# Performance work log

Measured on AMD Instinct MI355X. Metric: run time of the kernel, lower is better.

## Reference

```python
import jax, jax.numpy as jnp
import numpy as np

NF, D, H = 32, 256, 128  # n_features, d_model, d_model//2
B, T = 16, 512
EPS = 1e-5

def _ln(x, g, b):
    m = jnp.mean(x, axis=-1, keepdims=True)
    v = jnp.mean((x - m) ** 2, axis=-1, keepdims=True)
    return (x - m) * jax.lax.rsqrt(v + EPS) * g + b


def setup_inputs() -> dict:
    key = jax.random.key(0)
    ks = jax.random.split(key, 16)
    s = 0.05
    inp = {
        "x": jax.random.normal(ks[0], (B, T, NF), dtype=jnp.float32),
        # batched per-feature GRN params (d_in=1 -> fc1 weight is (NF,H))
        "w1": jax.random.normal(ks[1], (NF, H)) * s,
        "b1": jnp.zeros((NF, H)),
        "w2": jax.random.normal(ks[2], (NF, H, D)) * s,
        "b2": jnp.zeros((NF, D)),
        "wg": jax.random.normal(ks[3], (NF, H, D)) * s,
        "bg": jnp.zeros((NF, D)),
        "ws": jax.random.normal(ks[4], (NF, D)) * s,  # skip Linear(1,D)
        "bs": jnp.zeros((NF, D)),
        "ln_g": jnp.ones((NF, D)),
        "ln_b": jnp.zeros((NF, D)),
        # weight GRN: d_in=NF*D, d_hidden=D, d_out=NF
        "W1": jax.random.normal(ks[5], (NF * D, D)) * s,
        "B1": jnp.zeros((D,)),
        "W2": jax.random.normal(ks[6], (D, NF)) * s,
        "B2": jnp.zeros((NF,)),
        "Wg": jax.random.normal(ks[7], (D, NF)) * s,
        "Bg": jnp.zeros((NF,)),
        "Ws": jax.random.normal(ks[8], (NF * D, NF)) * s,
        "Bs": jnp.zeros((NF,)),
        "LN_g": jnp.ones((NF,)),
        "LN_b": jnp.zeros((NF,)),
    }
    return inp


def reference(x, w1, b1, w2, b2, wg, bg, ws, bs, ln_g, ln_b,
              W1, B1, W2, B2, Wg, Bg, Ws, Bs, LN_g, LN_b):
    Bn, Tn, Fn = x.shape
    # --- all per-feature GRNs batched over the feature axis (dropout=eval/identity) ---
    h = jax.nn.elu(x[..., None] * w1 + b1)                      # (B,T,F,H)
    proj = jnp.einsum('btfh,fhd->btfd', h, w2) + b2             # (B,T,F,D)
    gate = jax.nn.sigmoid(jnp.einsum('btfh,fhd->btfd', h, wg) + bg)
    skip = x[..., None] * ws + bs                               # (B,T,F,D)
    stacked = _ln(skip + gate * proj, ln_g, ln_b)               # (B,T,F,D)
    # --- softmax feature weights from mean-pooled flat features ---
    flat_pooled = stacked.mean(axis=1).reshape(Bn, Fn * stacked.shape[-1])  # (B,F*D)
    hw = jax.nn.elu(flat_pooled @ W1 + B1)                      # (B,D)
    pw = hw @ W2 + B2
    gw = jax.nn.sigmoid(hw @ Wg + Bg)
    wgrn = _ln(flat_pooled @ Ws + Bs + gw * pw, LN_g, LN_b)     # (B,F)
    weights = jax.nn.softmax(wgrn, axis=-1)                     # (B,F)
    # --- weighted feature combine ---
    selected = jnp.einsum('btfd,bf->btd', stacked, weights)     # (B,T,D)
    return selected, weights
```

## Files before the change

kernel.cpp:

```cpp
#include <hip/hip_runtime.h>
#include <hip/hip_fp16.h>

#define NF 32
#define DM 256
#define HH 128
#define BB 16
#define TT 512
#define BT 8192
#define OUT_W_OFF 2097152
#define EPS 1e-5f

typedef __bf16 bf16x8 __attribute__((ext_vector_type(8)));
typedef float  f32x16 __attribute__((ext_vector_type(16)));
typedef __fp16 f16x2 __attribute__((ext_vector_type(2)));
typedef __fp16 f16x8 __attribute__((ext_vector_type(8)));

__device__ __forceinline__ float eluf(float z){ return z > 0.f ? z : __expf(z) - 1.f; }
__device__ __forceinline__ float sigm(float z){ return 1.f/(1.f + __expf(-z)); }
__device__ __forceinline__ unsigned f2bf(float x){
  unsigned u = __float_as_uint(x);
  u += 0x7fffu + ((u>>16)&1u);
  return u>>16;
}

template<int MT, int NTHR>
__device__ __forceinline__ void build_A(uint4* Apack, const float* __restrict__ x,
                                        const float* __restrict__ w1, const float* __restrict__ b1,
                                        int f, int tok0, int tid){
  #pragma unroll
  for (int p = 0; p < (MT*512)/NTHR; ++p){
    int slot = tid + p*NTHR;
    int l  = slot & 63;
    int ks = (slot>>6)&7;
    int mt = slot>>9;
    int m  = mt*32 + (l&31);
    int k0 = ks*16 + (l>>5)*8;
    float xv = x[(tok0+m)*NF + f];
    const float* wp = w1 + f*HH + k0;
    const float* bp = b1 + f*HH + k0;
    float4 wa = *(const float4*)wp, wb = *(const float4*)(wp+4);
    float4 ba = *(const float4*)bp, bb = *(const float4*)(bp+4);
    bf16x8 v;
    v[0] = (__bf16)eluf(fmaf(xv, wa.x, ba.x));
    v[1] = (__bf16)eluf(fmaf(xv, wa.y, ba.y));
    v[2] = (__bf16)eluf(fmaf(xv, wa.z, ba.z));
    v[3] = (__bf16)eluf(fmaf(xv, wa.w, ba.w));
    v[4] = (__bf16)eluf(fmaf(xv, wb.x, bb.x));
    v[5] = (__bf16)eluf(fmaf(xv, wb.y, bb.y));
    v[6] = (__bf16)eluf(fmaf(xv, wb.z, bb.z));
    v[7] = (__bf16)eluf(fmaf(xv, wb.w, bb.w));
    Apack[slot] = __builtin_bit_cast(uint4, v);
  }
}

__global__ __launch_bounds__(256) void k_prep(const float* __restrict__ w2,
                                              const float* __restrict__ wgm,
                                              uint4* __restrict__ Wpk){
  __shared__ float ssrc[2][128][32];
  const int tid = threadIdx.x;
  const int f = blockIdx.x, c = blockIdx.y;
  #pragma unroll
  for (int it = 0; it < 32; ++it){
    int idx = tid + it*256;
    int arr = idx >> 12;
    int rem = idx & 4095;
    int k = rem >> 5, dd = rem & 31;
    const float* src = arr ? wgm : w2;
    ssrc[arr][k][dd] = src[(f*HH + k)*DM + c*32 + dd];
  }
  __syncthreads();
  #pragma unroll
  for (int p = 0; p < 4; ++p){
    int oc = tid + p*256;
    int nt = oc>>9, ks = (oc>>6)&7, l = oc&63;
    int k0 = ks*16 + (l>>5)*8, dd = l&31;
    float v[8];
    #pragma unroll
    for (int j=0;j<8;++j) v[j] = ssrc[nt][k0+j][dd];
    uint4 pk;
    pk.x = f2bf(v[0]) | (f2bf(v[1])<<16);
    pk.y = f2bf(v[2]) | (f2bf(v[3])<<16);
    pk.z = f2bf(v[4]) | (f2bf(v[5])<<16);
    pk.w = f2bf(v[6]) | (f2bf(v[7])<<16);
    Wpk[(f*8 + c)*1024 + oc] = pk;
  }
}

__global__ __launch_bounds__(512, 2) void k_pass1(const float* __restrict__ x,  const float* __restrict__ w1,
    const float* __restrict__ b1, const float* __restrict__ b2, const float* __restrict__ bg,
    const float* __restrict__ wsk, const float* __restrict__ bsk,
    const float* __restrict__ lng, const float* __restrict__ lnb,
    const uint4* __restrict__ Wpk,
    float* __restrict__ pooled, uint4* __restrict__ stk4){
  __shared__ uint4 smem[4096];
  __shared__ float xs[128];
  __shared__ float poolbuf[256];
  const int tid = threadIdx.x, lane = tid&63, wid = tid>>6;
  const int tt = wid>>1, ch = wid&1;
  const int col = lane&31, q = lane>>5;
  const int f = blockIdx.y;
  const int tok0 = blockIdx.x*128;
  const int b = tok0 >> 9;
  if (tid < 256) poolbuf[tid] = 0.f;
  if (tid < 128) xs[tid] = x[(tok0 + tid)*NF + f];

  build_A<4,512>(smem, x, w1, b1, f, tok0, tid);
  __syncthreads();
  bf16x8 afr[8];
  #pragma unroll
  for (int ks=0; ks<8; ++ks) afr[ks] = __builtin_bit_cast(bf16x8, smem[(tt*8+ks)*64 + lane]);
  __syncthreads();

  __fp16* stage = (__fp16*)smem;
  #pragma unroll 1
  for (int ci=0; ci<4; ++ci){
    const int c = ch*4 + ci;
    const uint4* wb = Wpk + (f*8 + c)*1024;
    bf16x8 bfr[8];
    #pragma unroll
    for (int ks=0;ks<8;++ks) bfr[ks] = __builtin_bit_cast(bf16x8, wb[ks*64 + lane]);
    f32x16 acc0 = {0.f};
    #pragma unroll
    for (int ks=0;ks<8;++ks) acc0 = __builtin_amdgcn_mfma_f32_32x32x16_bf16(afr[ks], bfr[ks], acc0, 0,0,0);
    __builtin_amdgcn_sched_barrier(0);
    #pragma unroll
    for (int ks=0;ks<8;++ks) bfr[ks] = __builtin_bit_cast(bf16x8, wb[512 + ks*64 + lane]);
    f32x16 acc1 = {0.f};
    #pragma unroll
    for (int ks=0;ks<8;++ks) acc1 = __builtin_amdgcn_mfma_f32_32x32x16_bf16(afr[ks], bfr[ks], acc1, 0,0,0);
    __builtin_amdgcn_sched_barrier(0);
    const int d = c*32 + col;
    const float b2v = b2[f*DM+d], bgv = bg[f*DM+d];
    #pragma unroll
    for (int i=0;i<8;++i){
      const int r0 = 2*i, r1 = r0+1;
      const int t0 = tt*32 + (r0&3) + 8*(i>>1) + 4*q;
      stage[ t0   *256 + d] = (__fp16)(sigm(acc1[r0]+bgv)*(acc0[r0]+b2v));
      stage[(t0+1)*256 + d] = (__fp16)(sigm(acc1[r1]+bgv)*(acc0[r1]+b2v));
    }
  }
  __syncthreads();

  const int oc = tid & 31;
  float4 ga = *(const float4*)(lng + f*DM + oc*8);
  float4 gb = *(const float4*)(lng + f*DM + oc*8 + 4);
  float4 la = *(const float4*)(lnb + f*DM + oc*8);
  float4 lb = *(const float4*)(lnb + f*DM + oc*8 + 4);
  float4 wa = *(const float4*)(wsk + f*DM + oc*8);
  float4 wbv = *(const float4*)(wsk + f*DM + oc*8 + 4);
  float4 sa = *(const float4*)(bsk + f*DM + oc*8);
  float4 sb = *(const float4*)(bsk + f*DM + oc*8 + 4);
  float gj[8] = {ga.x,ga.y,ga.z,ga.w,gb.x,gb.y,gb.z,gb.w};
  float bj[8] = {la.x,la.y,la.z,la.w,lb.x,lb.y,lb.z,lb.w};
  float wj[8] = {wa.x,wa.y,wa.z,wa.w,wbv.x,wbv.y,wbv.z,wbv.w};
  float cj[8] = {sa.x,sa.y,sa.z,sa.w,sb.x,sb.y,sb.z,sb.w};
  float ps[8];
  #pragma unroll
  for (int j=0;j<8;++j) ps[j]=0.f;
  #pragma unroll
  for (int p=0;p<8;++p){
    int slot = tid + p*512;
    int t = slot >> 5;
    uint4 v = smem[slot];
    f16x8 s8 = __builtin_bit_cast(f16x8, v);
    float xt = xs[t];
    float s[8];
    float ssum = 0.f, ssq = 0.f;
    #pragma unroll
    for (int j=0;j<8;++j){
      s[j] = fmaf(xt, wj[j], cj[j]) + (float)s8[j];
      ssum += s[j];
      ssq = fmaf(s[j], s[j], ssq);
    }
    ssum += __shfl_xor(ssum,1);  ssq += __shfl_xor(ssq,1);
    ssum += __shfl_xor(ssum,2);  ssq += __shfl_xor(ssq,2);
    ssum += __shfl_xor(ssum,4);  ssq += __shfl_xor(ssq,4);
    ssum += __shfl_xor(ssum,8);  ssq += __shfl_xor(ssq,8);
    ssum += __shfl_xor(ssum,16); ssq += __shfl_xor(ssq,16);
    float mu = ssum * (1.f/256.f);
    float var = fmaf(-mu, mu, ssq*(1.f/256.f));
    float rs = rsqrtf(fmaxf(var, 0.f) + EPS);
    float nmr = -mu*rs;
    float sh[8];
    #pragma unroll
    for (int j=0;j<8;++j){
      sh[j] = fmaf(fmaf(s[j], rs, nmr), gj[j], bj[j]);
      ps[j] += sh[j];
    }
    uint4 pk;
    pk.x = __builtin_bit_cast(unsigned, __builtin_amdgcn_cvt_pkrtz(sh[0], sh[1]));
    pk.y = __builtin_bit_cast(unsigned, __builtin_amdgcn_cvt_pkrtz(sh[2], sh[3]));
    pk.z = __builtin_bit_cast(unsigned, __builtin_amdgcn_cvt_pkrtz(sh[4], sh[5]));
    pk.w = __builtin_bit_cast(unsigned, __builtin_amdgcn_cvt_pkrtz(sh[6], sh[7]));
    stk4[(size_t)(tok0 + t)*1024 + (size_t)f*32 + oc] = pk;
  }
  #pragma unroll
  for (int j=0;j<8;++j) ps[j] += __shfl_xor(ps[j], 32);
  if (q == 0){
    #pragma unroll
    for (int j=0;j<8;++j) atomicAdd(&poolbuf[oc*8 + j], ps[j]);
  }
  __syncthreads();
  if (tid < 256) atomicAdd(&pooled[b*8192 + f*DM + tid], poolbuf[tid]);
}

__global__ __launch_bounds__(256) void k_pass2a(const float* __restrict__ pooled,
    const float* __restrict__ W1, const float* __restrict__ Wsm,
    float* __restrict__ hw_pre, float* __restrict__ sk_pre){
  __shared__ float fl[512];
  const int tid = threadIdx.x;
  const int b = blockIdx.x;
  const int k0 = blockIdx.y * 512;
  fl[tid]       = pooled[b*8192 + k0 + tid]       * (1.f/512.f);
  fl[tid+256]   = pooled[b*8192 + k0 + tid + 256] * (1.f/512.f);
  __syncthreads();
  float acc = 0.f;
  const float* wcol = W1 + (size_t)k0*DM + tid;
  #pragma unroll 4
  for (int i=0;i<512;++i) acc = fmaf(fl[i], wcol[(size_t)i*DM], acc);
  atomicAdd(&hw_pre[b*DM + tid], acc);
  const int colj = tid & 31, sub = tid >> 5;
  float acc2 = 0.f;
  const float* wscol = Wsm + (size_t)(k0 + sub*64)*NF + colj;
  const float* fls = fl + sub*64;
  #pragma unroll 4
  for (int i=0;i<64;++i) acc2 = fmaf(fls[i], wscol[(size_t)i*NF], acc2);
  atomicAdd(&sk_pre[b*NF + colj], acc2);
}

__global__ __launch_bounds__(64) void k_pass2b(const float* __restrict__ hw_pre, const float* __restrict__ sk_pre,
    const float* __restrict__ B1, const float* __restrict__ W2, const float* __restrict__ B2,
    const float* __restrict__ Wg, const float* __restrict__ Bg, const float* __restrict__ Bs,
    const float* __restrict__ LNg, const float* __restrict__ LNb,
    float* __restrict__ out, float* __restrict__ wsel){
  __shared__ float hw[256];
  const int tid = threadIdx.x, b = blockIdx.x;
  for (int i=tid;i<256;i+=64) hw[i] = eluf(hw_pre[b*DM+i] + B1[i]);
  __syncthreads();
  if (tid < 32){
    const int j = tid;
    float ap = B2[j], ag = Bg[j];
    #pragma unroll 4
    for (int i=0;i<256;++i){ float h = hw[i]; ap = fmaf(h, W2[i*NF+j], ap); ag = fmaf(h, Wg[i*NF+j], ag); }
    float gw = sigm(ag);
    float v = sk_pre[b*NF+j] + Bs[j] + gw*ap;
    float s1 = v;
    s1 += __shfl_xor(s1,1); s1 += __shfl_xor(s1,2); s1 += __shfl_xor(s1,4); s1 += __shfl_xor(s1,8); s1 += __shfl_xor(s1,16);
    float mean = s1*(1.f/32.f);
    float dv = v - mean;
    float s2 = dv*dv;
    s2 += __shfl_xor(s2,1); s2 += __shfl_xor(s2,2); s2 += __shfl_xor(s2,4); s2 += __shfl_xor(s2,8); s2 += __shfl_xor(s2,16);
    float wn = fmaf(dv * rsqrtf(s2*(1.f/32.f) + EPS), LNg[j], LNb[j]);
    float mx = wn;
    mx = fmaxf(mx, __shfl_xor(mx,1)); mx = fmaxf(mx, __shfl_xor(mx,2)); mx = fmaxf(mx, __shfl_xor(mx,4));
    mx = fmaxf(mx, __shfl_xor(mx,8)); mx = fmaxf(mx, __shfl_xor(mx,16));
    float e = __expf(wn - mx);
    float se = e;
    se += __shfl_xor(se,1); se += __shfl_xor(se,2); se += __shfl_xor(se,4); se += __shfl_xor(se,8); se += __shfl_xor(se,16);
    float wgt = e / se;
    out[OUT_W_OFF + b*NF + j] = wgt;
    wsel[b*NF + j] = wgt;
  }
}

__global__ __launch_bounds__(256) void k_comb(const uint4* __restrict__ stk4,
    const float* __restrict__ wsel, float* __restrict__ out){
  __shared__ float wloc[NF];
  const int tid = threadIdx.x, lane = tid&63;
  const int t = blockIdx.x*4 + (tid>>6);
  const int b = t >> 9;
  if (tid < NF) wloc[tid] = wsel[b*NF + tid];
  __syncthreads();
  const int oc = lane&31, fh = lane>>5;
  float acc[8];
  #pragma unroll
  for (int j=0;j<8;++j) acc[j]=0.f;
  #pragma unroll
  for (int j=0;j<16;++j){
    int f = fh*16 + j;
    uint4 v = stk4[(size_t)t*1024 + f*32 + oc];
    f16x8 hv = __builtin_bit_cast(f16x8, v);
    float wf = wloc[f];
    #pragma unroll
    for (int jj=0;jj<8;++jj) acc[jj] = fmaf(wf, (float)hv[jj], acc[jj]);
  }
  #pragma unroll
  for (int jj=0;jj<8;++jj) acc[jj] += __shfl_xor(acc[jj], 32);
  if (fh == 0){
    float4* o = (float4*)(out + (size_t)t*DM + oc*8);
    o[0] = make_float4(acc[0],acc[1],acc[2],acc[3]);
    o[1] = make_float4(acc[4],acc[5],acc[6],acc[7]);
  }
}

extern "C" void kernel_launch(void* const* d_in, const int* in_sizes, int n_in,
                              void* d_out, int out_size, void* d_ws, size_t ws_size,
                              hipStream_t stream) {
  const float* x   = (const float*)d_in[0];
  const float* w1  = (const float*)d_in[1];
  const float* b1  = (const float*)d_in[2];
  const float* w2  = (const float*)d_in[3];
  const float* b2  = (const float*)d_in[4];
  const float* wgm = (const float*)d_in[5];
  const float* bg  = (const float*)d_in[6];
  const float* wsk = (const float*)d_in[7];
  const float* bsk = (const float*)d_in[8];
  const float* lng = (const float*)d_in[9];
  const float* lnb = (const float*)d_in[10];
  const float* W1  = (const float*)d_in[11];
  const float* B1  = (const float*)d_in[12];
  const float* W2  = (const float*)d_in[13];
  const float* B2  = (const float*)d_in[14];
  const float* Wg  = (const float*)d_in[15];
  const float* Bg  = (const float*)d_in[16];
  const float* Wsm = (const float*)d_in[17];
  const float* Bs  = (const float*)d_in[18];
  const float* LNg = (const float*)d_in[19];
  const float* LNb = (const float*)d_in[20];
  float* out = (float*)d_out;

  char* ws = (char*)d_ws;
  uint4* Wpk    = (uint4*)ws;
  uint4* stk4   = (uint4*)(ws + 4194304);
  float* pooled = (float*)(ws + 138412032);
  float* hw_pre = (float*)(ws + 138936320);
  float* sk_pre = (float*)(ws + 138952704);
  float* wsel   = (float*)(ws + 138954752);

  (void)hipMemsetAsync(pooled, 0, 524288, stream);
  (void)hipMemsetAsync(hw_pre, 0, 16384 + 2048, stream);

  k_prep<<<dim3(32,8), 256, 0, stream>>>(w2, wgm, Wpk);
  k_pass1<<<dim3(64,32), 512, 0, stream>>>(x, w1, b1, b2, bg, wsk, bsk, lng, lnb,
                                           Wpk, pooled, stk4);
  k_pass2a<<<dim3(16,16), 256, 0, stream>>>(pooled, W1, Wsm, hw_pre, sk_pre);
  k_pass2b<<<16, 64, 0, stream>>>(hw_pre, sk_pre, B1, W2, B2, Wg, Bg, Bs, LNg, LNb, out, wsel);
  k_comb<<<2048, 256, 0, stream>>>(stk4, wsel, out);
}
```

Baseline: 295.4 us.

## Batch pass2a over all batches and interleave stacked layout by token groups

k_pass2a now has each block handle one 256-row slice of W1 for all 16 batch rows, so each W1 element is loaded once and reused across batches, where it was previously reread by every batch. The grid shrinks from 256 blocks to 32, which cuts parallelism. The stacked fp16 buffer is also relaid so the 4 tokens a k_comb block processes sit contiguously per feature, which changes the write pattern in pass1 and the read pattern in comb. The W1 reuse removes roughly 16x redundant weight traffic, but the kernel may become latency-bound with only 32 blocks.

After: 308.7 us. 1.04x slower.

```diff
diff --git a/kernel.cpp b/kernel.cpp
--- a/kernel.cpp
+++ b/kernel.cpp
@@ -192,7 +192,8 @@
     pk.y = __builtin_bit_cast(unsigned, __builtin_amdgcn_cvt_pkrtz(sh[2], sh[3]));
     pk.z = __builtin_bit_cast(unsigned, __builtin_amdgcn_cvt_pkrtz(sh[4], sh[5]));
     pk.w = __builtin_bit_cast(unsigned, __builtin_amdgcn_cvt_pkrtz(sh[6], sh[7]));
-    stk4[(size_t)(tok0 + t)*1024 + (size_t)f*32 + oc] = pk;
+    const int tg = tok0 + t;
+    stk4[(size_t)(tg>>2)*4096 + (size_t)f*128 + (size_t)(tg&3)*32 + oc] = pk;
   }
   #pragma unroll
   for (int j=0;j<8;++j) ps[j] += __shfl_xor(ps[j], 32);
@@ -207,25 +208,38 @@
 __global__ __launch_bounds__(256) void k_pass2a(const float* __restrict__ pooled,
     const float* __restrict__ W1, const float* __restrict__ Wsm,
     float* __restrict__ hw_pre, float* __restrict__ sk_pre){
-  __shared__ float fl[512];
+  __shared__ float fl[16][256];
   const int tid = threadIdx.x;
-  const int b = blockIdx.x;
-  const int k0 = blockIdx.y * 512;
-  fl[tid]       = pooled[b*8192 + k0 + tid]       * (1.f/512.f);
-  fl[tid+256]   = pooled[b*8192 + k0 + tid + 256] * (1.f/512.f);
-  __syncthreads();
-  float acc = 0.f;
+  const int k0 = blockIdx.x * 256;
+  #pragma unroll
+  for (int p = 0; p < 16; ++p){
+    int idx = tid + p*256;
+    int bb = idx >> 8, ii = idx & 255;
+    fl[bb][ii] = pooled[bb*8192 + k0 + ii] * (1.f/512.f);
+  }
+  __syncthreads();
+  float acc[16];
+  #pragma unroll
+  for (int b=0;b<16;++b) acc[b]=0.f;
   const float* wcol = W1 + (size_t)k0*DM + tid;
   #pragma unroll 4
-  for (int i=0;i<512;++i) acc = fmaf(fl[i], wcol[(size_t)i*DM], acc);
-  atomicAdd(&hw_pre[b*DM + tid], acc);
-  const int colj = tid & 31, sub = tid >> 5;
-  float acc2 = 0.f;
-  const float* wscol = Wsm + (size_t)(k0 + sub*64)*NF + colj;
-  const float* fls = fl + sub*64;
-  #pragma unroll 4
-  for (int i=0;i<64;++i) acc2 = fmaf(fls[i], wscol[(size_t)i*NF], acc2);
-  atomicAdd(&sk_pre[b*NF + colj], acc2);
+  for (int i=0;i<256;++i){
+    float w = wcol[(size_t)i*DM];
+    #pragma unroll
+    for (int b=0;b<16;++b) acc[b] = fmaf(fl[b][i], w, acc[b]);
+  }
+  #pragma unroll
+  for (int b=0;b<16;++b) atomicAdd(&hw_pre[b*DM + tid], acc[b]);
+  const int colj = tid & 31, bh = tid >> 5;
+  const float* wscol = Wsm + (size_t)k0*NF + colj;
+  #pragma unroll 1
+  for (int pass=0; pass<2; ++pass){
+    const int bb = bh + pass*8;
+    float a2 = 0.f;
+    #pragma unroll 4
+    for (int i=0;i<256;++i) a2 = fmaf(fl[bb][i], wscol[(size_t)i*NF], a2);
+    atomicAdd(&sk_pre[bb*NF + colj], a2);
+  }
 }
 
 __global__ __launch_bounds__(64) void k_pass2b(const float* __restrict__ hw_pre, const float* __restrict__ sk_pre,
@@ -267,7 +281,9 @@
     const float* __restrict__ wsel, float* __restrict__ out){
   __shared__ float wloc[NF];
   const int tid = threadIdx.x, lane = tid&63;
-  const int t = blockIdx.x*4 + (tid>>6);
+  const int tc = blockIdx.x;
+  const int ts = tid>>6;
+  const int t = tc*4 + ts;
   const int b = t >> 9;
   if (tid < NF) wloc[tid] = wsel[b*NF + tid];
   __syncthreads();
@@ -278,7 +294,7 @@
   #pragma unroll
   for (int j=0;j<16;++j){
     int f = fh*16 + j;
-    uint4 v = stk4[(size_t)t*1024 + f*32 + oc];
+    uint4 v = stk4[(size_t)tc*4096 + f*128 + ts*32 + oc];
     f16x8 hv = __builtin_bit_cast(f16x8, v);
     float wf = wloc[f];
     #pragma unroll
@@ -333,7 +349,7 @@
   k_prep<<<dim3(32,8), 256, 0, stream>>>(w2, wgm, Wpk);
   k_pass1<<<dim3(64,32), 512, 0, stream>>>(x, w1, b1, b2, bg, wsk, bsk, lng, lnb,
                                            Wpk, pooled, stk4);
-  k_pass2a<<<dim3(16,16), 256, 0, stream>>>(pooled, W1, Wsm, hw_pre, sk_pre);
+  k_pass2a<<<dim3(32), 256, 0, stream>>>(pooled, W1, Wsm, hw_pre, sk_pre);
   k_pass2b<<<16, 64, 0, stream>>>(hw_pre, sk_pre, B1, W2, B2, Wg, Bg, Bs, LNg, LNb, out, wsel);
   k_comb<<<2048, 256, 0, stream>>>(stk4, wsel, out);
 }
```

## Fold memsets into prep kernel, fuse pass2 via last-block counter, regroup stacked layout

Applied to the files above, without the earlier changes.

Replaces the two hipMemsetAsync calls by zeroing the accumulators inside k_prep, and merges k_pass2a and k_pass2b into one kernel where the last block to finish (tracked by an atomic counter) computes the softmax weights for all batches. Also changes the stacked fp16 buffer layout so four consecutive tokens for a feature are adjacent, so k_comb reads within a contiguous 64KB chunk per block. This removes two memset launches and one kernel launch. The cost is a serialized tail done by a single block and extra atomics.

New measurement: 325.7 us. 10.3% more time.

```diff
diff --git a/kernel.cpp b/kernel.cpp
--- a/kernel.cpp
+++ b/kernel.cpp
@@ -55,10 +55,23 @@
 
 __global__ __launch_bounds__(256) void k_prep(const float* __restrict__ w2,
                                               const float* __restrict__ wgm,
-                                              uint4* __restrict__ Wpk){
+                                              uint4* __restrict__ Wpk,
+                                              float* __restrict__ pooled,
+                                              float* __restrict__ hw_pre,
+                                              float* __restrict__ sk_pre,
+                                              unsigned* __restrict__ counter){
   __shared__ float ssrc[2][128][32];
   const int tid = threadIdx.x;
   const int f = blockIdx.x, c = blockIdx.y;
+  {
+    const int gb = blockIdx.y*gridDim.x + blockIdx.x;
+    const int gt = gb*256 + tid;
+    pooled[gt] = 0.f;
+    pooled[gt + 65536] = 0.f;
+    if (gt < 4096) hw_pre[gt] = 0.f;
+    else if (gt < 4608) sk_pre[gt - 4096] = 0.f;
+    if (gt == 0) *counter = 0u;
+  }
   #pragma unroll
   for (int it = 0; it < 32; ++it){
     int idx = tid + it*256;
@@ -192,7 +205,8 @@
     pk.y = __builtin_bit_cast(unsigned, __builtin_amdgcn_cvt_pkrtz(sh[2], sh[3]));
     pk.z = __builtin_bit_cast(unsigned, __builtin_amdgcn_cvt_pkrtz(sh[4], sh[5]));
     pk.w = __builtin_bit_cast(unsigned, __builtin_amdgcn_cvt_pkrtz(sh[6], sh[7]));
-    stk4[(size_t)(tok0 + t)*1024 + (size_t)f*32 + oc] = pk;
+    const int tg = tok0 + t;
+    stk4[(size_t)(tg>>2)*4096 + (size_t)f*128 + (size_t)(tg&3)*32 + oc] = pk;
   }
   #pragma unroll
   for (int j=0;j<8;++j) ps[j] += __shfl_xor(ps[j], 32);
@@ -204,10 +218,16 @@
   if (tid < 256) atomicAdd(&pooled[b*8192 + f*DM + tid], poolbuf[tid]);
 }
 
-__global__ __launch_bounds__(256) void k_pass2a(const float* __restrict__ pooled,
+__global__ __launch_bounds__(256) void k_pass2(const float* __restrict__ pooled,
     const float* __restrict__ W1, const float* __restrict__ Wsm,
-    float* __restrict__ hw_pre, float* __restrict__ sk_pre){
+    float* __restrict__ hw_pre, float* __restrict__ sk_pre,
+    const float* __restrict__ B1, const float* __restrict__ W2, const float* __restrict__ B2,
+    const float* __restrict__ Wg, const float* __restrict__ Bg, const float* __restrict__ Bs,
+    const float* __restrict__ LNg, const float* __restrict__ LNb,
+    unsigned* __restrict__ counter, float* __restrict__ out, float* __restrict__ wsel){
   __shared__ float fl[512];
+  __shared__ float hwt[16][256];
+  __shared__ int amLast;
   const int tid = threadIdx.x;
   const int b = blockIdx.x;
   const int k0 = blockIdx.y * 512;
@@ -226,24 +246,31 @@
   #pragma unroll 4
   for (int i=0;i<64;++i) acc2 = fmaf(fls[i], wscol[(size_t)i*NF], acc2);
   atomicAdd(&sk_pre[b*NF + colj], acc2);
-}
-
-__global__ __launch_bounds__(64) void k_pass2b(const float* __restrict__ hw_pre, const float* __restrict__ sk_pre,
-    const float* __restrict__ B1, const float* __restrict__ W2, const float* __restrict__ B2,
-    const float* __restrict__ Wg, const float* __restrict__ Bg, const float* __restrict__ Bs,
-    const float* __restrict__ LNg, const float* __restrict__ LNb,
-    float* __restrict__ out, float* __restrict__ wsel){
-  __shared__ float hw[256];
-  const int tid = threadIdx.x, b = blockIdx.x;
-  for (int i=tid;i<256;i+=64) hw[i] = eluf(hw_pre[b*DM+i] + B1[i]);
-  __syncthreads();
-  if (tid < 32){
-    const int j = tid;
+
+  __threadfence();
+  __syncthreads();
+  if (tid == 0){
+    unsigned old = atomicAdd(counter, 1u);
+    amLast = (old == 255u) ? 1 : 0;
+  }
+  __syncthreads();
+  if (!amLast) return;
+  #pragma unroll
+  for (int p=0;p<16;++p){
+    float v = atomicAdd(&hw_pre[p*DM + tid], 0.f);
+    hwt[p][tid] = eluf(v + B1[tid]);
+  }
+  __syncthreads();
+  const int j = tid & 31;
+  const int bl = tid >> 5;
+  #pragma unroll 1
+  for (int pass=0; pass<2; ++pass){
+    const int bb = bl + pass*8;
     float ap = B2[j], ag = Bg[j];
     #pragma unroll 4
-    for (int i=0;i<256;++i){ float h = hw[i]; ap = fmaf(h, W2[i*NF+j], ap); ag = fmaf(h, Wg[i*NF+j], ag); }
+    for (int i=0;i<256;++i){ float h = hwt[bb][i]; ap = fmaf(h, W2[i*NF+j], ap); ag = fmaf(h, Wg[i*NF+j], ag); }
     float gw = sigm(ag);
-    float v = sk_pre[b*NF+j] + Bs[j] + gw*ap;
+    float v = atomicAdd(&sk_pre[bb*NF + j], 0.f) + Bs[j] + gw*ap;
     float s1 = v;
     s1 += __shfl_xor(s1,1); s1 += __shfl_xor(s1,2); s1 += __shfl_xor(s1,4); s1 += __shfl_xor(s1,8); s1 += __shfl_xor(s1,16);
     float mean = s1*(1.f/32.f);
@@ -258,8 +285,8 @@
     float se = e;
     se += __shfl_xor(se,1); se += __shfl_xor(se,2); se += __shfl_xor(se,4); se += __shfl_xor(se,8); se += __shfl_xor(se,16);
     float wgt = e / se;
-    out[OUT_W_OFF + b*NF + j] = wgt;
-    wsel[b*NF + j] = wgt;
+    out[OUT_W_OFF + bb*NF + j] = wgt;
+    wsel[bb*NF + j] = wgt;
   }
 }
 
@@ -267,7 +294,9 @@
     const float* __restrict__ wsel, float* __restrict__ out){
   __shared__ float wloc[NF];
   const int tid = threadIdx.x, lane = tid&63;
-  const int t = blockIdx.x*4 + (tid>>6);
+  const int tc = blockIdx.x;
+  const int ts = tid>>6;
+  const int t = tc*4 + ts;
   const int b = t >> 9;
   if (tid < NF) wloc[tid] = wsel[b*NF + tid];
   __syncthreads();
@@ -278,7 +307,7 @@
   #pragma unroll
   for (int j=0;j<16;++j){
     int f = fh*16 + j;
-    uint4 v = stk4[(size_t)t*1024 + f*32 + oc];
+    uint4 v = stk4[(size_t)tc*4096 + f*128 + ts*32 + oc];
     f16x8 hv = __builtin_bit_cast(f16x8, v);
     float wf = wloc[f];
     #pragma unroll
@@ -320,20 +349,19 @@
   float* out = (float*)d_out;
 
   char* ws = (char*)d_ws;
-  uint4* Wpk    = (uint4*)ws;
-  uint4* stk4   = (uint4*)(ws + 4194304);
-  float* pooled = (float*)(ws + 138412032);
-  float* hw_pre = (float*)(ws + 138936320);
-  float* sk_pre = (float*)(ws + 138952704);
-  float* wsel   = (float*)(ws + 138954752);
-
-  (void)hipMemsetAsync(pooled, 0, 524288, stream);
-  (void)hipMemsetAsync(hw_pre, 0, 16384 + 2048, stream);
-
-  k_prep<<<dim3(32,8), 256, 0, stream>>>(w2, wgm, Wpk);
+  uint4* Wpk      = (uint4*)ws;
+  uint4* stk4     = (uint4*)(ws + 4194304);
+  float* pooled   = (float*)(ws + 138412032);
+  float* hw_pre   = (float*)(ws + 138936320);
+  float* sk_pre   = (float*)(ws + 138952704);
+  float* wsel     = (float*)(ws + 138954752);
+  unsigned* cnt   = (unsigned*)(ws + 138956800);
+
+  k_prep<<<dim3(32,8), 256, 0, stream>>>(w2, wgm, Wpk, pooled, hw_pre, sk_pre, cnt);
   k_pass1<<<dim3(64,32), 512, 0, stream>>>(x, w1, b1, b2, bg, wsk, bsk, lng, lnb,
                                            Wpk, pooled, stk4);
-  k_pass2a<<<dim3(16,16), 256, 0, stream>>>(pooled, W1, Wsm, hw_pre, sk_pre);
-  k_pass2b<<<16, 64, 0, stream>>>(hw_pre, sk_pre, B1, W2, B2, Wg, Bg, Bs, LNg, LNb, out, wsel);
+  k_pass2<<<dim3(16,16), 256, 0, stream>>>(pooled, W1, Wsm, hw_pre, sk_pre,
+                                           B1, W2, B2, Wg, Bg, Bs, LNg, LNb,
+                                           cnt, out, wsel);
   k_comb<<<2048, 256, 0, stream>>>(stk4, wsel, out);
 }
```
